# Kernel tuning notes

Hardware: AMD Instinct MI355X
Metric: run time of the kernel (lower is better)

The kernel has to match this reference:

```python
import jax, jax.numpy as jnp
import numpy as np


def setup_inputs() -> dict:
    key = jax.random.key(0)
    # frames: stack of 4 feature maps, each [B, C, H, W]
    frames = jax.random.normal(key, (4, 8, 64, 160, 160), dtype=jnp.float32)
    return {"frames": frames}


def reference(frames) -> jnp.ndarray:
    # frames: [4, B, C, H, W]
    B, C = frames.shape[1], frames.shape[2]
    # V = cat(x1..x4, dim=1) -> [B, 4C, H, W]
    V = jnp.concatenate([frames[i] for i in range(4)], axis=1)
    outs = []
    for i in range(4):
        # Qi = cat([xi]*4, dim=1) -> [B, 4C, H, W]
        Qi = jnp.tile(frames[i], (1, 4, 1, 1))
        # softmax over the 4C channel axis, then gate V
        s = jax.nn.softmax(Qi * V, axis=1) * V  # [B, 4C, H, W]
        # chunk into 4 blocks of C channels and sum -> [B, C, H, W]
        outs.append(s.reshape(B, 4, C, *s.shape[2:]).sum(axis=1))
    return jnp.concatenate(outs, axis=1)  # [B, 4C, H, W]
```

## Files before the change

kernel.cpp:

```cpp
#include <hip/hip_runtime.h>


#define HW 25600
#define NP 32
#define ROW 257
#define TILES_PER_B 800
#define TPB 4
#define BLOCKS_PER_B 200

typedef float f32x4 __attribute__((ext_vector_type(4)));

__device__ __forceinline__ float wave_allsum(float x) {
  int v;
  v = __builtin_amdgcn_update_dpp(0, __float_as_int(x), 0xB1, 0xf, 0xf, true);
  x += __int_as_float(v);
  v = __builtin_amdgcn_update_dpp(0, __float_as_int(x), 0x4E, 0xf, 0xf, true);
  x += __int_as_float(v);
  v = __builtin_amdgcn_update_dpp(0, __float_as_int(x), 0x141, 0xf, 0xf, true);
  x += __int_as_float(v);
  v = __builtin_amdgcn_update_dpp(0, __float_as_int(x), 0x140, 0xf, 0xf, true);
  x += __int_as_float(v);
  v = __builtin_amdgcn_update_dpp(0, __float_as_int(x), 0x142, 0xa, 0xf, false);
  x += __int_as_float(v);
  v = __builtin_amdgcn_update_dpp(0, __float_as_int(x), 0x143, 0xc, 0xf, false);
  x += __int_as_float(v);
  return __int_as_float(__builtin_amdgcn_readlane(__float_as_int(x), 63));
}

__global__ __launch_bounds__(256, 4) void fused_frame_softmax(
    const float* __restrict__ in, float* __restrict__ out) {
  __shared__ float Xs[NP * ROW];

  const int b     = blockIdx.x / BLOCKS_PER_B;
  const int pbase = (blockIdx.x % BLOCKS_PER_B) * (TPB * NP);
  const int t     = threadIdx.x;


  f32x4 pf[8];

  #pragma unroll
  for (int it = 0; it < 8; ++it) {
    const int q  = it * 256 + t;
    const int ch = q >> 3;
    const int pq = (q & 7) << 2;
    const int off = ((ch >> 6) * 512 + b * 64 + (ch & 63)) * HW + pbase + pq;
    pf[it] = __builtin_nontemporal_load(
        reinterpret_cast<const f32x4*>(in + off));
  }
  #pragma unroll
  for (int it = 0; it < 8; ++it) {
    const int q  = it * 256 + t;
    const int ch = q >> 3;
    const int pq = (q & 7) << 2;
    Xs[(pq + 0) * ROW + ch] = pf[it].x;
    Xs[(pq + 1) * ROW + ch] = pf[it].y;
    Xs[(pq + 2) * ROW + ch] = pf[it].z;
    Xs[(pq + 3) * ROW + ch] = pf[it].w;
  }
  __syncthreads();

  const int lane  = t & 63;
  const int wbase = (t >> 6) * 8;

  for (int k = 0; k < TPB; ++k) {
    if (k + 1 < TPB) {
      #pragma unroll
      for (int it = 0; it < 8; ++it) {
        const int q  = it * 256 + t;
        const int ch = q >> 3;
        const int pq = (q & 7) << 2;
        const int off =
            ((ch >> 6) * 512 + b * 64 + (ch & 63)) * HW + pbase + (k + 1) * NP + pq;
        pf[it] = __builtin_nontemporal_load(
            reinterpret_cast<const f32x4*>(in + off));
      }
    }

    #pragma unroll 2
    for (int pp = 0; pp < 8; ++pp) {
      float* row = Xs + (wbase + pp) * ROW;
      const float x0 = row[lane];
      const float x1 = row[lane + 64];
      const float x2 = row[lane + 128];
      const float x3 = row[lane + 192];

      const float E00 = __expf(x0 * x0);
      const float E01 = __expf(x0 * x1);
      const float E02 = __expf(x0 * x2);
      const float E03 = __expf(x0 * x3);
      const float E11 = __expf(x1 * x1);
      const float E12 = __expf(x1 * x2);
      const float E13 = __expf(x1 * x3);
      const float E22 = __expf(x2 * x2);
      const float E23 = __expf(x2 * x3);
      const float E33 = __expf(x3 * x3);

      const float z0 = wave_allsum(E00 + E01 + E02 + E03);
      const float z1 = wave_allsum(E01 + E11 + E12 + E13);
      const float z2 = wave_allsum(E02 + E12 + E22 + E23);
      const float z3 = wave_allsum(E03 + E13 + E23 + E33);

      const float r0 = __builtin_amdgcn_rcpf(z0);
      const float r1 = __builtin_amdgcn_rcpf(z1);
      const float r2 = __builtin_amdgcn_rcpf(z2);
      const float r3 = __builtin_amdgcn_rcpf(z3);

      row[lane]       = (E00 * x0 + E01 * x1 + E02 * x2 + E03 * x3) * r0;
      row[lane + 64]  = (E01 * x0 + E11 * x1 + E12 * x2 + E13 * x3) * r1;
      row[lane + 128] = (E02 * x0 + E12 * x1 + E22 * x2 + E23 * x3) * r2;
      row[lane + 192] = (E03 * x0 + E13 * x1 + E23 * x2 + E33 * x3) * r3;
    }
    __syncthreads();

    #pragma unroll
    for (int it = 0; it < 8; ++it) {
      const int q  = it * 256 + t;
      const int ch = q >> 3;
      const int pq = (q & 7) << 2;
      f32x4 v;
      v.x = Xs[(pq + 0) * ROW + ch];
      v.y = Xs[(pq + 1) * ROW + ch];
      v.z = Xs[(pq + 2) * ROW + ch];
      v.w = Xs[(pq + 3) * ROW + ch];
      if (k + 1 < TPB) {
        Xs[(pq + 0) * ROW + ch] = pf[it].x;
        Xs[(pq + 1) * ROW + ch] = pf[it].y;
        Xs[(pq + 2) * ROW + ch] = pf[it].z;
        Xs[(pq + 3) * ROW + ch] = pf[it].w;
      }
      const int ooff = (b * 256 + ch) * HW + pbase + k * NP + pq;
      __builtin_nontemporal_store(v, reinterpret_cast<f32x4*>(out + ooff));
    }
    __syncthreads();
  }
}

extern "C" void kernel_launch(void* const* d_in, const int* in_sizes, int n_in,
                              void* d_out, int out_size, void* d_ws, size_t ws_size,
                              hipStream_t stream) {
  const float* in = (const float*)d_in[0];
  float* out      = (float*)d_out;
  fused_frame_softmax<<<dim3(8 * BLOCKS_PER_B), dim3(256), 0, stream>>>(in, out);
}
```

Before: 344.3 us.

## Use 512-thread blocks and deepen global-load prefetch pipeline

Doubles the block size to 512 threads so each thread moves half as many vectors per tile and each wave handles four pixel rows instead of eight. It also restructures the prefetch so the load for tile k+2 is issued right after tile k+1 is written to shared memory, which keeps loads in flight during the compute phase. The goal is more memory-level parallelism and higher occupancy for this bandwidth-bound kernel. The cost is register pressure under the new launch bounds and more threads contending at each barrier.

```diff
diff --git a/kernel.cpp b/kernel.cpp
--- a/kernel.cpp
+++ b/kernel.cpp
@@ -4,9 +4,10 @@
 #define HW 25600
 #define NP 32
 #define ROW 257
-#define TILES_PER_B 800
 #define TPB 4
 #define BLOCKS_PER_B 200
+#define NTH 512
+#define SIT 4
 
 typedef float f32x4 __attribute__((ext_vector_type(4)));
 
@@ -27,7 +28,7 @@
   return __int_as_float(__builtin_amdgcn_readlane(__float_as_int(x), 63));
 }
 
-__global__ __launch_bounds__(256, 4) void fused_frame_softmax(
+__global__ __launch_bounds__(NTH, 6) void fused_frame_softmax(
     const float* __restrict__ in, float* __restrict__ out) {
   __shared__ float Xs[NP * ROW];
 
@@ -36,20 +37,19 @@
   const int t     = threadIdx.x;
 
 
-  f32x4 pf[8];
+  f32x4 pf[SIT];
 
   #pragma unroll
-  for (int it = 0; it < 8; ++it) {
-    const int q  = it * 256 + t;
+  for (int it = 0; it < SIT; ++it) {
+    const int q  = it * NTH + t;
     const int ch = q >> 3;
     const int pq = (q & 7) << 2;
     const int off = ((ch >> 6) * 512 + b * 64 + (ch & 63)) * HW + pbase + pq;
-    pf[it] = __builtin_nontemporal_load(
-        reinterpret_cast<const f32x4*>(in + off));
+    pf[it] = __builtin_nontemporal_load(reinterpret_cast<const f32x4*>(in + off));
   }
   #pragma unroll
-  for (int it = 0; it < 8; ++it) {
-    const int q  = it * 256 + t;
+  for (int it = 0; it < SIT; ++it) {
+    const int q  = it * NTH + t;
     const int ch = q >> 3;
     const int pq = (q & 7) << 2;
     Xs[(pq + 0) * ROW + ch] = pf[it].x;
@@ -59,25 +59,22 @@
   }
   __syncthreads();
 
+  #pragma unroll
+  for (int it = 0; it < SIT; ++it) {
+    const int q  = it * NTH + t;
+    const int ch = q >> 3;
+    const int pq = (q & 7) << 2;
+    const int off = ((ch >> 6) * 512 + b * 64 + (ch & 63)) * HW + pbase + NP + pq;
+    pf[it] = __builtin_nontemporal_load(reinterpret_cast<const f32x4*>(in + off));
+  }
+
   const int lane  = t & 63;
-  const int wbase = (t >> 6) * 8;
+  const int wbase = (t >> 6) * 4;
 
+  #pragma unroll
   for (int k = 0; k < TPB; ++k) {
-    if (k + 1 < TPB) {
-      #pragma unroll
-      for (int it = 0; it < 8; ++it) {
-        const int q  = it * 256 + t;
-        const int ch = q >> 3;
-        const int pq = (q & 7) << 2;
-        const int off =
-            ((ch >> 6) * 512 + b * 64 + (ch & 63)) * HW + pbase + (k + 1) * NP + pq;
-        pf[it] = __builtin_nontemporal_load(
-            reinterpret_cast<const f32x4*>(in + off));
-      }
-    }
-
     #pragma unroll 2
-    for (int pp = 0; pp < 8; ++pp) {
+    for (int pp = 0; pp < 4; ++pp) {
       float* row = Xs + (wbase + pp) * ROW;
       const float x0 = row[lane];
       const float x1 = row[lane + 64];
@@ -113,8 +110,8 @@
     __syncthreads();
 
     #pragma unroll
-    for (int it = 0; it < 8; ++it) {
-      const int q  = it * 256 + t;
+    for (int it = 0; it < SIT; ++it) {
+      const int q  = it * NTH + t;
       const int ch = q >> 3;
       const int pq = (q & 7) << 2;
       f32x4 v;
@@ -128,6 +125,12 @@
         Xs[(pq + 2) * ROW + ch] = pf[it].z;
         Xs[(pq + 3) * ROW + ch] = pf[it].w;
       }
+      if (k + 2 < TPB) {
+        const int off =
+            ((ch >> 6) * 512 + b * 64 + (ch & 63)) * HW + pbase + (k + 2) * NP + pq;
+        pf[it] = __builtin_nontemporal_load(
+            reinterpret_cast<const f32x4*>(in + off));
+      }
       const int ooff = (b * 256 + ch) * HW + pbase + k * NP + pq;
       __builtin_nontemporal_store(v, reinterpret_cast<f32x4*>(out + ooff));
     }
@@ -140,5 +143,5 @@
                               hipStream_t stream) {
   const float* in = (const float*)d_in[0];
   float* out      = (float*)d_out;
-  fused_frame_softmax<<<dim3(8 * BLOCKS_PER_B), dim3(256), 0, stream>>>(in, out);
+  fused_frame_softmax<<<dim3(8 * BLOCKS_PER_B), dim3(NTH), 0, stream>>>(in, out);
 }
```

New measurement: 346.2 us. No clear change (+0.5%).
